# Kernel optimization log

Measured on AMD Instinct MI355X. Metric: run time of the kernel, lower is better.

## Reference

```python
import jax, jax.numpy as jnp
import numpy as np

N, D_IN, D_OUT, E = 100000, 64, 64, 800000
C_IN, C_OUT = 1.0, 1.0
MAX_NORM = 1e6   # manifold.max_norm clamp used by PseudoHypAgg
EPS = 1e-15
BALL_EPS = 4e-3  # Poincare-ball projection margin (fp32)


def _artanh(x):
    return jnp.arctanh(jnp.clip(x, -1 + 1e-7, 1 - 1e-7))


def _proj(x, c):
    # project onto the open Poincare ball of curvature c
    sqrt_c = jnp.sqrt(c)
    norm = jnp.clip(jnp.linalg.norm(x, axis=-1, keepdims=True), EPS)
    maxn = (1.0 - BALL_EPS) / sqrt_c
    return jnp.where(norm > maxn, x / norm * maxn, x)


def _expmap0(u, c):
    sqrt_c = jnp.sqrt(c)
    n = jnp.clip(jnp.linalg.norm(u, axis=-1, keepdims=True), EPS)
    return jnp.tanh(sqrt_c * n) * u / (sqrt_c * n)


def _logmap0(p, c):
    sqrt_c = jnp.sqrt(c)
    n = jnp.clip(jnp.linalg.norm(p, axis=-1, keepdims=True), EPS)
    return _artanh(sqrt_c * n) * p / (sqrt_c * n)


def _mobius_add(x, y, c):
    x2 = jnp.sum(x * x, -1, keepdims=True)
    y2 = jnp.sum(y * y, -1, keepdims=True)
    xy = jnp.sum(x * y, -1, keepdims=True)
    num = (1 + 2 * c * xy + c * y2) * x + (1 - c * x2) * y
    den = 1 + 2 * c * xy + c * c * x2 * y2
    return num / jnp.clip(den, EPS)


def _mobius_matvec(M, x, c):
    sqrt_c = jnp.sqrt(c)
    x_norm = jnp.clip(jnp.linalg.norm(x, axis=-1, keepdims=True), EPS)
    mx = x @ M.T  # [N, D_OUT]
    mx_norm = jnp.clip(jnp.linalg.norm(mx, axis=-1, keepdims=True), EPS)
    res = jnp.tanh(mx_norm / x_norm * _artanh(sqrt_c * x_norm)) * mx / (mx_norm * sqrt_c)
    zero = jnp.all(mx == 0, axis=-1, keepdims=True)
    return jnp.where(zero, jnp.zeros_like(res), res)


def setup_inputs() -> dict:
    key = jax.random.key(0)
    k1, k2, k3, k4, k5, k6 = jax.random.split(key, 6)
    # node features: small-norm points inside the unit ball
    x = _proj(0.05 * jax.random.normal(k1, (N, D_IN), jnp.float32), C_IN)
    W = jax.random.normal(k2, (D_OUT, D_IN), jnp.float32) / np.float32(np.sqrt(D_IN))
    b = 0.01 * jax.random.normal(k3, (D_OUT,), jnp.float32)
    edge_row = jax.random.randint(k4, (E,), 0, N, jnp.int32)
    edge_col = jax.random.randint(k5, (E,), 0, N, jnp.int32)
    edge_val = jax.random.uniform(k6, (E,), jnp.float32) / 16.0  # ~normalized adj weights
    return {"x": x, "W": W, "b": b, "edge_row": edge_row,
            "edge_col": edge_col, "edge_val": edge_val}


def reference(x, W, b, edge_row, edge_col, edge_val):
    # --- PseudoHypLinear (eval mode: dropout inactive) ---
    mv = _mobius_matvec(W, x, C_IN)
    res = _proj(mv, C_IN)
    hyp_b = _proj(_expmap0(b[None, :], C_IN), C_IN)  # proj_tan0 is identity on the ball
    h = _proj(_mobius_add(res, hyp_b, C_IN), C_IN)
    # --- PseudoHypAgg (use_att=False): spmm in tangent space at origin ---
    x_t = _logmap0(h, C_IN)                              # [N, D_OUT]
    msg = edge_val[:, None] * x_t[edge_col]              # [E, D_OUT]
    support_t = jax.ops.segment_sum(msg, edge_row, num_segments=N)
    support_t = jnp.minimum(support_t, MAX_NORM)         # clamp(max=manifold.max_norm)
    h = _proj(_expmap0(support_t, C_IN), C_IN)           # proj_tan0 identity
    # --- PseudoHypAct: act in tangent at origin (c_in), re-embed with c_out ---
    xt = jax.nn.relu(_logmap0(h, C_IN))
    return _proj(_expmap0(xt, C_OUT), C_OUT)
```

## Files before the change

### kernel.cpp

```cpp
#include <hip/hip_runtime.h>
#include <hip/hip_fp16.h>
#include <math.h>

#define DD 64
#define BK 128
#define BCAP 2048
#define NBKT_MAX 800
#define CHUNK 8192
constexpr float FEPS = 1e-15f;
constexpr float MAXN = 1.0f - 4e-3f;

typedef _Float16 f16x8 __attribute__((ext_vector_type(8)));
typedef float f32x4 __attribute__((ext_vector_type(4)));

__device__ __forceinline__ float wsum(float v) {
    v += __shfl_xor(v, 32);
    v += __shfl_xor(v, 16);
    v += __shfl_xor(v, 8);
    v += __shfl_xor(v, 4);
    v += __shfl_xor(v, 2);
    v += __shfl_xor(v, 1);
    return v;
}

__device__ __forceinline__ int wave_incl_scan(int v) {
    int lane = threadIdx.x & 63;
    #pragma unroll
    for (int d = 1; d < 64; d <<= 1) {
        int t = __shfl_up(v, d);
        if (lane >= d) v += t;
    }
    return v;
}

__device__ __forceinline__ float artanh_c(float x) {
    x = fminf(fmaxf(x, -1.f + 1e-7f), 1.f - 1e-7f);
    return 0.5f * logf((1.f + x) / (1.f - x));
}

__global__ __launch_bounds__(512) void kfused(
    const float* __restrict__ x, const float* __restrict__ W,
    const float* __restrict__ bvec, __half* __restrict__ xth,
    const int* __restrict__ erow, const int* __restrict__ ecol,
    const float* __restrict__ eval_, int* __restrict__ gcnt,
    int2* __restrict__ binned, int nbkt, int n_edges, int n_nodes, int nbB) {
    const int t = threadIdx.x;

    if ((int)blockIdx.x < nbB) {
        __shared__ int lcnt[NBKT_MAX];
        __shared__ int goff[NBKT_MAX];
        const int eb = blockIdx.x * CHUNK;
        for (int i = t; i < nbkt; i += 512) lcnt[i] = 0;
        __syncthreads();
        int rk[16];
        #pragma unroll
        for (int i = 0; i < 16; ++i) {
            int e = eb + i * 512 + t;
            rk[i] = -1;
            if (e < n_edges) {
                int r = erow[e];
                int bkt = r >> 7;
                int rank = atomicAdd(&lcnt[bkt], 1);
                rk[i] = (bkt << 20) | ((r & (BK - 1)) << 13) | rank;
            }
        }
        __syncthreads();
        for (int i = t; i < nbkt; i += 512) {
            int c = lcnt[i];
            if (c > 0) goff[i] = atomicAdd(&gcnt[i], c);
        }
        __syncthreads();
        #pragma unroll
        for (int i = 0; i < 16; ++i) {
            int e = eb + i * 512 + t;
            if (e >= n_edges) continue;
            int bkt = rk[i] >> 20, lr = (rk[i] >> 13) & 127, rank = rk[i] & 8191;
            int pos = goff[bkt] + rank;
            if (pos < BCAP)
                binned[(size_t)bkt * BCAP + pos] =
                    make_int2((lr << 17) | ecol[e], __float_as_int(eval_[e]));
        }
        return;
    }

    const int lane = t & 63;
    const int wv = t >> 6;
    const int nw = ((int)blockIdx.x - nbB) * 128 + wv * 16;
    if (nw >= n_nodes) return;
    const int r16 = lane & 15;
    const int khi = lane >> 4;

    float bv = bvec[lane];
    float bn2 = wsum(bv * bv);
    float bn = fmaxf(sqrtf(bn2), FEPS);
    float bth = tanhf(bn);
    float p = bth * (bv / bn);
    float pnrm = bth * (sqrtf(bn2) / bn);
    float pn_c = fmaxf(pnrm, FEPS);
    if (pn_c > MAXN) p *= MAXN / pn_c;
    float y2 = wsum(p * p);
    float hbj[4];
    #pragma unroll
    for (int jt = 0; jt < 4; ++jt)
        hbj[jt] = __shfl(p, jt * 16 + r16);

    int nodeA = nw + r16;
    int nca = (nodeA < n_nodes) ? nodeA : (n_nodes - 1);
    const float* xrow = x + (size_t)nca * DD + khi * 8;
    f16x8 a[2];
    float xpart = 0.f;
    #pragma unroll
    for (int kc = 0; kc < 2; ++kc) {
        float4 v0 = *reinterpret_cast<const float4*>(xrow + kc * 32);
        float4 v1 = *reinterpret_cast<const float4*>(xrow + kc * 32 + 4);
        xpart += v0.x * v0.x + v0.y * v0.y + v0.z * v0.z + v0.w * v0.w
               + v1.x * v1.x + v1.y * v1.y + v1.z * v1.z + v1.w * v1.w;
        a[kc][0] = (_Float16)v0.x; a[kc][1] = (_Float16)v0.y;
        a[kc][2] = (_Float16)v0.z; a[kc][3] = (_Float16)v0.w;
        a[kc][4] = (_Float16)v1.x; a[kc][5] = (_Float16)v1.y;
        a[kc][6] = (_Float16)v1.z; a[kc][7] = (_Float16)v1.w;
    }
    xpart += __shfl_xor(xpart, 16);
    xpart += __shfl_xor(xpart, 32);
    float xn2d[4];
    #pragma unroll
    for (int r = 0; r < 4; ++r)
        xn2d[r] = __shfl(xpart, khi * 4 + r);

    f16x8 bfr[4][2];
    #pragma unroll
    for (int jt = 0; jt < 4; ++jt) {
        const float* wrow = W + (size_t)(jt * 16 + r16) * DD + khi * 8;
        #pragma unroll
        for (int kc = 0; kc < 2; ++kc) {
            float4 v0 = *reinterpret_cast<const float4*>(wrow + kc * 32);
            float4 v1 = *reinterpret_cast<const float4*>(wrow + kc * 32 + 4);
            bfr[jt][kc][0] = (_Float16)v0.x; bfr[jt][kc][1] = (_Float16)v0.y;
            bfr[jt][kc][2] = (_Float16)v0.z; bfr[jt][kc][3] = (_Float16)v0.w;
            bfr[jt][kc][4] = (_Float16)v1.x; bfr[jt][kc][5] = (_Float16)v1.y;
            bfr[jt][kc][6] = (_Float16)v1.z; bfr[jt][kc][7] = (_Float16)v1.w;
        }
    }

    f32x4 d[4];
    #pragma unroll
    for (int jt = 0; jt < 4; ++jt) {
        d[jt] = (f32x4){0.f, 0.f, 0.f, 0.f};
        #pragma unroll
        for (int kc = 0; kc < 2; ++kc)
            d[jt] = __builtin_amdgcn_mfma_f32_16x16x32_f16(a[kc], bfr[jt][kc], d[jt], 0, 0, 0);
    }

    float mx2p[4], mxhp[4];
    #pragma unroll
    for (int r = 0; r < 4; ++r) {
        float s2 = 0.f, sh = 0.f;
        #pragma unroll
        for (int jt = 0; jt < 4; ++jt) {
            s2 = fmaf(d[jt][r], d[jt][r], s2);
            sh = fmaf(d[jt][r], hbj[jt], sh);
        }
        mx2p[r] = s2; mxhp[r] = sh;
    }
    #pragma unroll
    for (int m = 1; m < 16; m <<= 1) {
        #pragma unroll
        for (int r = 0; r < 4; ++r) {
            mx2p[r] += __shfl_xor(mx2p[r], m);
            mxhp[r] += __shfl_xor(mxhp[r], m);
        }
    }

    float As[4], Bs[4];
    #pragma unroll
    for (int r = 0; r < 4; ++r) {
        float mx2 = mx2p[r], mxh = mxhp[r];
        float xn = fmaxf(sqrtf(xn2d[r]), FEPS);
        float mxn = fmaxf(sqrtf(mx2), FEPS);
        float th = tanhf((mxn / xn) * artanh_c(xn));
        float sres = (mx2 == 0.f) ? 0.f : th / mxn;
        float rn = (mx2 == 0.f) ? 0.f : th * (sqrtf(mx2) / mxn);
        float rn_c = fmaxf(rn, FEPS);
        float s1 = (rn_c > MAXN) ? sres * (MAXN / rn_c) : sres;
        float x2r = s1 * s1 * mx2;
        float xy = s1 * mxh;
        float ca = 1.f + 2.f * xy + y2;
        float cb = 1.f - x2r;
        float rden = 1.f / fmaxf(1.f + 2.f * xy + x2r * y2, FEPS);
        float al = ca * s1 * rden;
        float be = cb * rden;
        float h2 = al * al * mx2 + 2.f * al * be * mxh + be * be * y2;
        float hn = fmaxf(sqrtf(h2), FEPS);
        float sh = 1.f;
        if (hn > MAXN) { sh = MAXN / hn; hn = MAXN; }
        float su = sh * (artanh_c(hn) / hn);
        As[r] = su * al;
        Bs[r] = su * be;
    }

    #pragma unroll
    for (int r = 0; r < 4; ++r) {
        int node = nw + khi * 4 + r;
        if (node >= n_nodes) continue;
        #pragma unroll
        for (int jt = 0; jt < 4; ++jt) {
            float u = fmaf(As[r], d[jt][r], Bs[r] * hbj[jt]);
            xth[(size_t)node * DD + jt * 16 + r16] = __float2half_rn(u);
        }
    }
}

__device__ __forceinline__ void agg_epilogue(
    float4 acc, int row, int fl, float* __restrict__ out) {
    float4 s;
    s.x = fminf(acc.x, 1e6f); s.y = fminf(acc.y, 1e6f);
    s.z = fminf(acc.z, 1e6f); s.w = fminf(acc.w, 1e6f);
    float4 rs;
    rs.x = fmaxf(s.x, 0.f); rs.y = fmaxf(s.y, 0.f);
    rs.z = fmaxf(s.z, 0.f); rs.w = fmaxf(s.w, 0.f);
    float n2p = s.x * s.x + s.y * s.y + s.z * s.z + s.w * s.w;
    float sp2p = rs.x * rs.x + rs.y * rs.y + rs.z * rs.z + rs.w * rs.w;
    #pragma unroll
    for (int m = 1; m < 16; m <<= 1) {
        n2p += __shfl_xor(n2p, m);
        sp2p += __shfl_xor(sp2p, m);
    }
    float n = fmaxf(sqrtf(n2p), FEPS);
    float th = tanhf(n);
    float c1 = th / n;
    float pn = th * (sqrtf(n2p) / n);
    float pn_c = fmaxf(pn, FEPS);
    if (pn_c > MAXN) { c1 *= MAXN / pn_c; pn_c = MAXN; }
    float k1 = (artanh_c(pn_c) / pn_c) * c1;
    float u2 = k1 * k1 * sp2p;
    float un = fmaxf(sqrtf(u2), FEPS);
    float t2 = tanhf(un);
    float k2 = (t2 / un) * k1;
    float on = t2 * (sqrtf(u2) / un);
    float on_c = fmaxf(on, FEPS);
    if (on_c > MAXN) k2 *= MAXN / on_c;
    float4 o;
    o.x = k2 * rs.x; o.y = k2 * rs.y; o.z = k2 * rs.z; o.w = k2 * rs.w;
    reinterpret_cast<float4*>(out)[(size_t)row * 16 + fl] = o;
}

__global__ __launch_bounds__(512) void kagg2(
    const int* __restrict__ gcnt, const int2* __restrict__ binned,
    const __half* __restrict__ xth, float* __restrict__ out, int n_nodes) {
    __shared__ int hist[BK], offs[BK], cur[BK];
    __shared__ int2 srt[BCAP];
    const int t = threadIdx.x;
    const int b = blockIdx.x;
    for (int i = t; i < BK; i += 512) hist[i] = 0;
    __syncthreads();
    const int nrec = min(gcnt[b], BCAP);
    const int2* rec = binned + (size_t)b * BCAP;
    int2 rc[BCAP / 512];
    #pragma unroll
    for (int i = 0; i < BCAP / 512; ++i) {
        int j = i * 512 + t;
        if (j < nrec) {
            rc[i] = rec[j];
            atomicAdd(&hist[rc[i].x >> 17], 1);
        }
    }
    __syncthreads();
    if (t < 64) {
        int v = hist[t];
        int s = wave_incl_scan(v);
        offs[t] = s - v;
    }
    __syncthreads();
    if (t < 64) {
        int c = offs[63] + hist[63];
        int v = hist[64 + t];
        int s = wave_incl_scan(v);
        offs[64 + t] = c + s - v;
    }
    __syncthreads();
    for (int i = t; i < BK; i += 512) cur[i] = offs[i];
    __syncthreads();
    #pragma unroll
    for (int i = 0; i < BCAP / 512; ++i) {
        int j = i * 512 + t;
        if (j < nrec) {
            int lr = rc[i].x >> 17;
            int p = atomicAdd(&cur[lr], 1);
            srt[p] = make_int2(rc[i].x & 0x1FFFF, rc[i].y);
        }
    }
    __syncthreads();

    const int g = t >> 4, fl = t & 15;
    #pragma unroll
    for (int it = 0; it < BK / 32; ++it) {
        int lr = it * 32 + g;
        int row = b * BK + lr;
        if (row >= n_nodes) continue;
        int beg = offs[lr], end = beg + hist[lr];
        float4 acc = make_float4(0.f, 0.f, 0.f, 0.f);
        int j = beg;
        for (; j + 7 < end; j += 8) {
            int2 e[8];
            float2 r[8];
            #pragma unroll
            for (int q = 0; q < 8; ++q) e[q] = srt[j + q];
            #pragma unroll
            for (int q = 0; q < 8; ++q)
                r[q] = *reinterpret_cast<const float2*>(
                    xth + (size_t)e[q].x * DD + fl * 4);
            #pragma unroll
            for (int q = 0; q < 8; ++q) {
                float wq = __int_as_float(e[q].y);
                float2 lo = __half22float2(*reinterpret_cast<__half2*>(&r[q].x));
                float2 hi = __half22float2(*reinterpret_cast<__half2*>(&r[q].y));
                acc.x = fmaf(wq, lo.x, acc.x); acc.y = fmaf(wq, lo.y, acc.y);
                acc.z = fmaf(wq, hi.x, acc.z); acc.w = fmaf(wq, hi.y, acc.w);
            }
        }
        for (; j + 3 < end; j += 4) {
            int2 e[4];
            float2 r[4];
            #pragma unroll
            for (int q = 0; q < 4; ++q) e[q] = srt[j + q];
            #pragma unroll
            for (int q = 0; q < 4; ++q)
                r[q] = *reinterpret_cast<const float2*>(
                    xth + (size_t)e[q].x * DD + fl * 4);
            #pragma unroll
            for (int q = 0; q < 4; ++q) {
                float wq = __int_as_float(e[q].y);
                float2 lo = __half22float2(*reinterpret_cast<__half2*>(&r[q].x));
                float2 hi = __half22float2(*reinterpret_cast<__half2*>(&r[q].y));
                acc.x = fmaf(wq, lo.x, acc.x); acc.y = fmaf(wq, lo.y, acc.y);
                acc.z = fmaf(wq, hi.x, acc.z); acc.w = fmaf(wq, hi.y, acc.w);
            }
        }
        for (; j < end; ++j) {
            int2 e = srt[j];
            float2 r0 = *reinterpret_cast<const float2*>(
                xth + (size_t)e.x * DD + fl * 4);
            float w0 = __int_as_float(e.y);
            float2 lo = __half22float2(*reinterpret_cast<__half2*>(&r0.x));
            float2 hi = __half22float2(*reinterpret_cast<__half2*>(&r0.y));
            acc.x = fmaf(w0, lo.x, acc.x); acc.y = fmaf(w0, lo.y, acc.y);
            acc.z = fmaf(w0, hi.x, acc.z); acc.w = fmaf(w0, hi.y, acc.w);
        }
        agg_epilogue(acc, row, fl, out);
    }
}

extern "C" void kernel_launch(void* const* d_in, const int* in_sizes, int n_in,
                              void* d_out, int out_size, void* d_ws, size_t ws_size,
                              hipStream_t stream) {
    const float* x     = (const float*)d_in[0];
    const float* W     = (const float*)d_in[1];
    const float* b     = (const float*)d_in[2];
    const int*   erow  = (const int*)d_in[3];
    const int*   ecol  = (const int*)d_in[4];
    const float* eval_ = (const float*)d_in[5];
    const int n_nodes = in_sizes[0] / DD;
    const int n_edges = in_sizes[3];
    float* out = (float*)d_out;

    const int NBKT = (n_nodes + BK - 1) / BK;

    int2*   binned = (int2*)d_ws;
    __half* xth    = (__half*)(binned + (size_t)NBKT * BCAP);
    int*    gcnt   = (int*)(xth + (size_t)n_nodes * DD);

    const int nbB = (n_edges + CHUNK - 1) / CHUNK;
    const int nbL = (n_nodes + 127) / 128;

    hipMemsetAsync(gcnt, 0, NBKT_MAX * sizeof(int), stream);
    kfused<<<nbB + nbL, 512, 0, stream>>>(x, W, b, xth, erow, ecol, eval_,
                                          gcnt, binned, NBKT, n_edges, n_nodes, nbB);
    kagg2<<<NBKT, 512, 0, stream>>>(gcnt, binned, xth, out, n_nodes);
}
```

Measured before the change: 145.7 us.

## Pad bucket counters, double binning chunk, dedupe per-row math, use fast tanh/log

Binning blocks now each process 16384 edges instead of 8192, and the rank/bucket packing is widened to fit. Global bucket counters are padded with a stride of 16 ints so atomics from different buckets fall on separate cache lines. In the linear stage, each row's scalar hyperbolic math is done once per lane and broadcast with shuffles, rather than repeated four times per lane. Library tanhf/logf are replaced by __expf/__logf-based versions, trading some accuracy for cheaper transcendentals. The larger chunk halves the number of binning blocks and uses more registers per thread, so parallelism drops.

```diff
diff --git a/kernel.cpp b/kernel.cpp
--- a/kernel.cpp
+++ b/kernel.cpp
@@ -6,7 +6,8 @@
 #define BK 128
 #define BCAP 2048
 #define NBKT_MAX 800
-#define CHUNK 8192
+#define GSTRIDE 16
+#define CHUNK 16384
 constexpr float FEPS = 1e-15f;
 constexpr float MAXN = 1.0f - 4e-3f;
 
@@ -33,9 +34,15 @@
     return v;
 }
 
+__device__ __forceinline__ float tanh_fast(float x) {
+    float xc = fminf(x, 15.f);
+    float e = __expf(2.f * xc);
+    return (e - 1.f) / (e + 1.f);
+}
+
 __device__ __forceinline__ float artanh_c(float x) {
     x = fminf(fmaxf(x, -1.f + 1e-7f), 1.f - 1e-7f);
-    return 0.5f * logf((1.f + x) / (1.f - x));
+    return 0.5f * __logf((1.f + x) / (1.f - x));
 }
 
 __global__ __launch_bounds__(512) void kfused(
@@ -52,29 +59,29 @@
         const int eb = blockIdx.x * CHUNK;
         for (int i = t; i < nbkt; i += 512) lcnt[i] = 0;
         __syncthreads();
-        int rk[16];
-        #pragma unroll
-        for (int i = 0; i < 16; ++i) {
+        int rk[32];
+        #pragma unroll
+        for (int i = 0; i < 32; ++i) {
             int e = eb + i * 512 + t;
             rk[i] = -1;
             if (e < n_edges) {
                 int r = erow[e];
                 int bkt = r >> 7;
                 int rank = atomicAdd(&lcnt[bkt], 1);
-                rk[i] = (bkt << 20) | ((r & (BK - 1)) << 13) | rank;
+                rk[i] = (bkt << 21) | ((r & (BK - 1)) << 14) | rank;
             }
         }
         __syncthreads();
         for (int i = t; i < nbkt; i += 512) {
             int c = lcnt[i];
-            if (c > 0) goff[i] = atomicAdd(&gcnt[i], c);
+            if (c > 0) goff[i] = atomicAdd(&gcnt[i * GSTRIDE], c);
         }
         __syncthreads();
         #pragma unroll
-        for (int i = 0; i < 16; ++i) {
+        for (int i = 0; i < 32; ++i) {
             int e = eb + i * 512 + t;
             if (e >= n_edges) continue;
-            int bkt = rk[i] >> 20, lr = (rk[i] >> 13) & 127, rank = rk[i] & 8191;
+            int bkt = rk[i] >> 21, lr = (rk[i] >> 14) & 127, rank = rk[i] & 16383;
             int pos = goff[bkt] + rank;
             if (pos < BCAP)
                 binned[(size_t)bkt * BCAP + pos] =
@@ -93,7 +100,7 @@
     float bv = bvec[lane];
     float bn2 = wsum(bv * bv);
     float bn = fmaxf(sqrtf(bn2), FEPS);
-    float bth = tanhf(bn);
+    float bth = tanh_fast(bn);
     float p = bth * (bv / bn);
     float pnrm = bth * (sqrtf(bn2) / bn);
     float pn_c = fmaxf(pnrm, FEPS);
@@ -122,10 +129,6 @@
     }
     xpart += __shfl_xor(xpart, 16);
     xpart += __shfl_xor(xpart, 32);
-    float xn2d[4];
-    #pragma unroll
-    for (int r = 0; r < 4; ++r)
-        xn2d[r] = __shfl(xpart, khi * 4 + r);
 
     f16x8 bfr[4][2];
     #pragma unroll
@@ -171,31 +174,43 @@
         }
     }
 
+    const int idx16 = r16;
+    const int srcq = (idx16 >> 2) * 16;
+    float m0 = __shfl(mx2p[0], srcq), m1 = __shfl(mx2p[1], srcq);
+    float m2 = __shfl(mx2p[2], srcq), m3 = __shfl(mx2p[3], srcq);
+    float h0 = __shfl(mxhp[0], srcq), h1 = __shfl(mxhp[1], srcq);
+    float h2s = __shfl(mxhp[2], srcq), h3 = __shfl(mxhp[3], srcq);
+    int rr = idx16 & 3;
+    float mx2 = (rr == 0) ? m0 : (rr == 1) ? m1 : (rr == 2) ? m2 : m3;
+    float mxh = (rr == 0) ? h0 : (rr == 1) ? h1 : (rr == 2) ? h2s : h3;
+    float xn2c = __shfl(xpart, idx16);
+
+    float xn = fmaxf(sqrtf(xn2c), FEPS);
+    float mxn = fmaxf(sqrtf(mx2), FEPS);
+    float th = tanh_fast((mxn / xn) * artanh_c(xn));
+    float sres = (mx2 == 0.f) ? 0.f : th / mxn;
+    float rn = (mx2 == 0.f) ? 0.f : th * (sqrtf(mx2) / mxn);
+    float rn_c = fmaxf(rn, FEPS);
+    float s1 = (rn_c > MAXN) ? sres * (MAXN / rn_c) : sres;
+    float x2r = s1 * s1 * mx2;
+    float xy = s1 * mxh;
+    float ca = 1.f + 2.f * xy + y2;
+    float cb = 1.f - x2r;
+    float rden = 1.f / fmaxf(1.f + 2.f * xy + x2r * y2, FEPS);
+    float al = ca * s1 * rden;
+    float be = cb * rden;
+    float hh2 = al * al * mx2 + 2.f * al * be * mxh + be * be * y2;
+    float hn = fmaxf(sqrtf(hh2), FEPS);
+    float sh = 1.f;
+    if (hn > MAXN) { sh = MAXN / hn; hn = MAXN; }
+    float su = sh * (artanh_c(hn) / hn);
+    float Aone = su * al, Bone = su * be;
+
     float As[4], Bs[4];
     #pragma unroll
     for (int r = 0; r < 4; ++r) {
-        float mx2 = mx2p[r], mxh = mxhp[r];
-        float xn = fmaxf(sqrtf(xn2d[r]), FEPS);
-        float mxn = fmaxf(sqrtf(mx2), FEPS);
-        float th = tanhf((mxn / xn) * artanh_c(xn));
-        float sres = (mx2 == 0.f) ? 0.f : th / mxn;
-        float rn = (mx2 == 0.f) ? 0.f : th * (sqrtf(mx2) / mxn);
-        float rn_c = fmaxf(rn, FEPS);
-        float s1 = (rn_c > MAXN) ? sres * (MAXN / rn_c) : sres;
-        float x2r = s1 * s1 * mx2;
-        float xy = s1 * mxh;
-        float ca = 1.f + 2.f * xy + y2;
-        float cb = 1.f - x2r;
-        float rden = 1.f / fmaxf(1.f + 2.f * xy + x2r * y2, FEPS);
-        float al = ca * s1 * rden;
-        float be = cb * rden;
-        float h2 = al * al * mx2 + 2.f * al * be * mxh + be * be * y2;
-        float hn = fmaxf(sqrtf(h2), FEPS);
-        float sh = 1.f;
-        if (hn > MAXN) { sh = MAXN / hn; hn = MAXN; }
-        float su = sh * (artanh_c(hn) / hn);
-        As[r] = su * al;
-        Bs[r] = su * be;
+        As[r] = __shfl(Aone, khi * 4 + r);
+        Bs[r] = __shfl(Bone, khi * 4 + r);
     }
 
     #pragma unroll
@@ -226,7 +241,7 @@
         sp2p += __shfl_xor(sp2p, m);
     }
     float n = fmaxf(sqrtf(n2p), FEPS);
-    float th = tanhf(n);
+    float th = tanh_fast(n);
     float c1 = th / n;
     float pn = th * (sqrtf(n2p) / n);
     float pn_c = fmaxf(pn, FEPS);
@@ -234,7 +249,7 @@
     float k1 = (artanh_c(pn_c) / pn_c) * c1;
     float u2 = k1 * k1 * sp2p;
     float un = fmaxf(sqrtf(u2), FEPS);
-    float t2 = tanhf(un);
+    float t2 = tanh_fast(un);
     float k2 = (t2 / un) * k1;
     float on = t2 * (sqrtf(u2) / un);
     float on_c = fmaxf(on, FEPS);
@@ -253,7 +268,7 @@
     const int b = blockIdx.x;
     for (int i = t; i < BK; i += 512) hist[i] = 0;
     __syncthreads();
-    const int nrec = min(gcnt[b], BCAP);
+    const int nrec = min(gcnt[b * GSTRIDE], BCAP);
     const int2* rec = binned + (size_t)b * BCAP;
     int2 rc[BCAP / 512];
     #pragma unroll
@@ -372,7 +387,7 @@
     const int nbB = (n_edges + CHUNK - 1) / CHUNK;
     const int nbL = (n_nodes + 127) / 128;
 
-    hipMemsetAsync(gcnt, 0, NBKT_MAX * sizeof(int), stream);
+    hipMemsetAsync(gcnt, 0, NBKT_MAX * GSTRIDE * sizeof(int), stream);
     kfused<<<nbB + nbL, 512, 0, stream>>>(x, W, b, xth, erow, ecol, eval_,
                                           gcnt, binned, NBKT, n_edges, n_nodes, nbB);
     kagg2<<<NBKT, 512, 0, stream>>>(gcnt, binned, xth, out, n_nodes);
```

Result: slower. 149.7 us (+2.7%).
